# Performance work log

Hardware: AMD Instinct MI355X
Metric: run time of the kernel (lower is better)

Reference implementation:

```python
import jax, jax.numpy as jnp
import numpy as np


def setup_inputs() -> dict:
    key = jax.random.key(0)
    k1, k2 = jax.random.split(key)
    inputs = jax.random.normal(k1, (16, 4096, 512), dtype=jnp.float32)
    # torch init is uniform(-1/num_codes, 1/num_codes); match scale
    codebooks = jax.random.uniform(k2, (4, 1024, 512), dtype=jnp.float32,
                                   minval=-1.0 / 1024, maxval=1.0 / 1024)
    return {"inputs": inputs, "codebooks": codebooks}


def _vq_level(flat, codebook):
    # flat: [N, D], codebook: [K, D]
    dists = (jnp.sum(flat * flat, axis=1, keepdims=True)
             + jnp.sum(codebook * codebook, axis=1)
             - 2.0 * jnp.matmul(flat, codebook.T))  # [N, K]
    idx = jnp.argmin(dists, axis=1)                  # [N]
    quantized = codebook[idx]                         # [N, D]
    return quantized, idx


def reference(inputs, codebooks):
    sg = jax.lax.stop_gradient
    num_levels = codebooks.shape[0]
    shp = inputs.shape
    D = shp[-1]
    flat_in = inputs.reshape(-1, D)

    residual = flat_in
    total_q = jnp.zeros_like(flat_in)
    all_idx = []
    total_q_loss = jnp.float32(0.0)
    total_e_loss = jnp.float32(0.0)
    for lvl in range(num_levels):
        quantized, idx = _vq_level(residual, codebooks[lvl])
        q_loss = jnp.mean((quantized - sg(residual)) ** 2)
        e_loss = jnp.mean((sg(quantized) - residual) ** 2)
        all_idx.append(idx.reshape(shp[:-1]))
        total_q = total_q + quantized
        total_q_loss = total_q_loss + q_loss
        total_e_loss = total_e_loss + e_loss
        residual = residual - sg(quantized)

    total_q = total_q.reshape(shp)
    final_ste = inputs + sg(total_q - inputs)
    return (final_ste,
            total_q_loss / num_levels,
            total_e_loss / num_levels,
            jnp.stack(all_idx, axis=0))
```

## Files before the change

kernel.cpp:

```cpp
#include <hip/hip_runtime.h>


#define NROWS 65536
#define DDIM  512
#define KC    1024

#define AS1 __attribute__((address_space(1)))
#define AS3 __attribute__((address_space(3)))

typedef __attribute__((ext_vector_type(8))) short short8v;
typedef __attribute__((ext_vector_type(4))) float f32x4;

__device__ __forceinline__ unsigned short f2bf(float f) {
  unsigned u = __float_as_uint(f);
  unsigned r = (u + 0x7FFFu + ((u >> 16) & 1u)) >> 16;
  return (unsigned short)r;
}

__device__ __forceinline__ bool lexlt(float v1, int i1, float v2, int i2) {
  return (v1 < v2) || (v1 == v2 && i1 < i2);
}

__device__ __forceinline__ void merge3(float& v0, float& v1, float& v2,
                                       float m0, float m1, float m2) {
  float x1 = fmaxf(v0, m0); v0 = fminf(v0, m0);
  float y = fminf(v1, m1), z = fmaxf(v1, m1);
  float nv1 = fminf(x1, y);
  v2 = fminf(fmaxf(x1, y), fminf(z, fminf(v2, m2)));
  v1 = nv1;
}

__device__ __forceinline__ void top3of4(float k0, float k1, float k2, float k3,
                                        float& m0, float& m1, float& m2) {
  float a = fminf(k0, k1), b = fmaxf(k0, k1);
  float c = fminf(k2, k3), d = fmaxf(k2, k3);
  m0 = fminf(a, c);
  float f = fmaxf(a, c), g = fminf(b, d);
  m1 = fminf(f, g); m2 = fmaxf(f, g);
}

__device__ __forceinline__ void wg_barrier() {
  asm volatile("" ::: "memory");
  __builtin_amdgcn_s_barrier();
  asm volatile("" ::: "memory");
}


__global__ void cnorm_kernel(const float* __restrict__ cbs,
                             float* __restrict__ cn32) {
  const int code = blockIdx.x;
  const int l = threadIdx.x;
  if (l >= 32) return;
  const int b = l >> 3, j = l & 7;
  const float* p = cbs + (size_t)code * DDIM + b * 128 + j;
  float racc;
  {
    #pragma clang fp contract(off)
    float x0 = p[0];
    racc = x0 * x0;
    for (int s = 1; s < 16; ++s) { float x = p[8 * s]; float sq = x * x; racc = racc + sq; }
  }
  {
    #pragma clang fp contract(off)
    float o;
    o = __shfl_xor(racc, 1, 64);  racc = racc + o;
    o = __shfl_xor(racc, 2, 64);  racc = racc + o;
    o = __shfl_xor(racc, 4, 64);  racc = racc + o;
    o = __shfl_xor(racc, 8, 64);  racc = racc + o;
    o = __shfl_xor(racc, 16, 64); racc = racc + o;
    if (l == 0) cn32[code] = racc;
  }
}

__global__ void cvt_bf16_kernel(const float4* __restrict__ in4,
                                ushort4* __restrict__ o4, long n4) {
  for (long i = blockIdx.x * (long)blockDim.x + threadIdx.x; i < n4;
       i += (long)gridDim.x * blockDim.x) {
    float4 v = in4[i];
    ushort4 o; o.x = f2bf(v.x); o.y = f2bf(v.y); o.z = f2bf(v.z); o.w = f2bf(v.w);
    o4[i] = o;
  }
}

__global__ void __launch_bounds__(256)
resupd_kernel(const float4* __restrict__ x4, const float* __restrict__ cbs,
              const float* __restrict__ idx_f, ushort4* __restrict__ res4,
              int nlev) {
  const int gwave = (blockIdx.x * 256 + threadIdx.x) >> 6;
  const int lane  = threadIdx.x & 63;
  const int nwaves = gridDim.x * 4;
  const float4* cb4 = (const float4*)cbs;
  for (int row = gwave; row < NROWS; row += nwaves) {
    int ci[4];
    for (int l = 0; l < nlev; ++l) ci[l] = (int)idx_f[(size_t)l * NROWS + row];
    #pragma unroll
    for (int half = 0; half < 2; ++half) {
      const int p = half * 64 + lane;
      float4 v = x4[(size_t)row * 128 + p];
      for (int l = 0; l < nlev; ++l) {
        const float4 c = cb4[((size_t)(l * KC + ci[l])) * 128 + p];
        v.x -= c.x; v.y -= c.y; v.z -= c.z; v.w -= c.w;
      }
      ushort4 o; o.x = f2bf(v.x); o.y = f2bf(v.y); o.z = f2bf(v.z); o.w = f2bf(v.w);
      res4[(size_t)row * 128 + p] = o;
    }
  }
}

template <int LVL>
__global__ void __launch_bounds__(256, 4)
score_gemm(const ushort* __restrict__ res, const ushort* __restrict__ cbb,
           const float* __restrict__ cn32, float* __restrict__ partials) {
  __shared__ ushort At[2][128 * 32];
  __shared__ ushort Bt[2][128 * 32];
  __shared__ float halfTop[2][2][64][3];

  const int t = threadIdx.x;
  const int w = t >> 6, lane = t & 63;
  const int fr = lane & 15, kg = lane >> 4;
  const int rh = w >> 1, ch = w & 1;
  const int xcd = blockIdx.x & 7;
  const int j   = blockIdx.x >> 3;
  const int colTile = j & 7;
  const int rowTile = xcd * 64 + (j >> 3);
  const int row0 = rowTile * 128;

  const ushort* Asrc = res + (size_t)row0 * DDIM;
  const ushort* Bsrc = cbb + ((size_t)LVL * KC + colTile * 128) * DDIM;

  const int r0s = t >> 2, kq = t & 3;
  const int r1s = 64 + r0s;
  const size_t off0 = (size_t)r0s * DDIM + (size_t)((kq ^ (r0s & 3)) * 8);
  const size_t off1 = (size_t)r1s * DDIM + (size_t)((kq ^ (r1s & 3)) * 8);
  const int kgs = (kg ^ (fr & 3)) * 8;

  f32x4 acc[4][4];
  #pragma unroll
  for (int ri = 0; ri < 4; ++ri)
    #pragma unroll
    for (int ci = 0; ci < 4; ++ci) { f32x4 z = {0.f, 0.f, 0.f, 0.f}; acc[ri][ci] = z; }

#define STG(KS, BI)                                                           \
  do {                                                                        \
    __builtin_amdgcn_global_load_lds(                                         \
        (const AS1 unsigned*)(Asrc + off0 + (KS) * 32),                       \
        (AS3 unsigned*)&At[BI][w * 512], 16, 0, 0);                           \
    __builtin_amdgcn_global_load_lds(                                         \
        (const AS1 unsigned*)(Asrc + off1 + (KS) * 32),                       \
        (AS3 unsigned*)&At[BI][2048 + w * 512], 16, 0, 0);                    \
    __builtin_amdgcn_global_load_lds(                                         \
        (const AS1 unsigned*)(Bsrc + off0 + (KS) * 32),                       \
        (AS3 unsigned*)&Bt[BI][w * 512], 16, 0, 0);                           \
    __builtin_amdgcn_global_load_lds(                                         \
        (const AS1 unsigned*)(Bsrc + off1 + (KS) * 32),                       \
        (AS3 unsigned*)&Bt[BI][2048 + w * 512], 16, 0, 0);                    \
  } while (0)

  STG(0, 0);
  #pragma unroll
  for (int ks = 0; ks < 16; ++ks) {
    const int cur = ks & 1;
    if (ks < 15) {
      STG(ks + 1, !cur);
      asm volatile("s_waitcnt vmcnt(4)" ::: "memory");
    } else {
      asm volatile("s_waitcnt vmcnt(0)" ::: "memory");
    }
    wg_barrier();
    short8v a[4], b[4];
    #pragma unroll
    for (int i = 0; i < 4; ++i)
      a[i] = *(const short8v*)&At[cur][(rh * 64 + i * 16 + fr) * 32 + kgs];
    #pragma unroll
    for (int i = 0; i < 4; ++i)
      b[i] = *(const short8v*)&Bt[cur][(ch * 64 + i * 16 + fr) * 32 + kgs];
    __builtin_amdgcn_s_setprio(1);
    #pragma unroll
    for (int ri = 0; ri < 4; ++ri)
      #pragma unroll
      for (int ci = 0; ci < 4; ++ci)
        acc[ri][ci] = __builtin_amdgcn_mfma_f32_16x16x32_bf16(
            a[ri], b[ci], acc[ri][ci], 0, 0, 0);
    __builtin_amdgcn_s_setprio(0);
    wg_barrier();
  }
#undef STG

  float cnv[4];
  #pragma unroll
  for (int ci = 0; ci < 4; ++ci)
    cnv[ci] = cn32[LVL * KC + colTile * 128 + ch * 64 + ci * 16 + fr] + 0.25f;

  #pragma unroll
  for (int ri = 0; ri < 4; ++ri) {
    #pragma unroll
    for (int j2 = 0; j2 < 4; ++j2) {
      float k[4];
      #pragma unroll
      for (int ci = 0; ci < 4; ++ci) {
        float s = fmaf(-2.0f, acc[ri][ci][j2], cnv[ci]);
        unsigned col = (unsigned)(colTile * 128 + ch * 64 + ci * 16 + fr);
        unsigned u = (__float_as_uint(s) & 0xFFFFFC00u) | col;
        k[ci] = __uint_as_float(u);
      }
      float m0, m1, m2;
      top3of4(k[0], k[1], k[2], k[3], m0, m1, m2);
      #pragma unroll
      for (int m = 1; m <= 8; m <<= 1) {
        float t0 = __shfl_xor(m0, m, 64);
        float t1 = __shfl_xor(m1, m, 64);
        float t2 = __shfl_xor(m2, m, 64);
        merge3(m0, m1, m2, t0, t1, t2);
      }
      if (fr == 0) {
        int row64 = ri * 16 + kg * 4 + j2;
        halfTop[rh][ch][row64][0] = m0;
        halfTop[rh][ch][row64][1] = m1;
        halfTop[rh][ch][row64][2] = m2;
      }
    }
  }
  __syncthreads();

  if (t < 128) {
    const int lrh = t >> 6, r64 = t & 63;
    float u0 = halfTop[lrh][0][r64][0], u1 = halfTop[lrh][0][r64][1],
          u2 = halfTop[lrh][0][r64][2];
    float s0 = halfTop[lrh][1][r64][0], s1 = halfTop[lrh][1][r64][1],
          s2 = halfTop[lrh][1][r64][2];
    merge3(u0, u1, u2, s0, s1, s2);
    const int grow = row0 + lrh * 64 + r64;
    partials[(size_t)(colTile * 3 + 0) * NROWS + grow] = u0;
    partials[(size_t)(colTile * 3 + 1) * NROWS + grow] = u1;
    partials[(size_t)(colTile * 3 + 2) * NROWS + grow] = u2;
  }
}

__global__ void __launch_bounds__(256)
combine_kernel(const float* __restrict__ partials, float* __restrict__ idx_io,
               int* __restrict__ qcnt, int* __restrict__ qrows,
               int* __restrict__ qcand, int LVL) {
  const int row = blockIdx.x * 256 + threadIdx.x;
  float v0 = 3.4e38f, v1 = 3.4e38f, v2 = 3.4e38f, v3 = 3.4e38f;
  #pragma unroll
  for (int p = 0; p < 24; ++p) {
    const float kv = partials[(size_t)p * NROWS + row];
    const bool b3 = kv < v3, b2 = kv < v2, b1 = kv < v1, b0 = kv < v0;
    v3 = b3 ? (b2 ? v2 : kv) : v3;
    v2 = b2 ? (b1 ? v1 : kv) : v2;
    v1 = b1 ? (b0 ? v0 : kv) : v1;
    v0 = b0 ? kv : v0;
  }
  if (v1 - v0 > 1e-3f) {
    idx_io[(size_t)LVL * NROWS + row] = (float)(__float_as_uint(v0) & 1023u);
  } else {
    int pos = atomicAdd(qcnt, 1);
    qrows[pos] = row;
    qcand[pos * 4 + 0] = (int)(__float_as_uint(v0) & 1023u);
    qcand[pos * 4 + 1] = (int)(__float_as_uint(v1) & 1023u);
    qcand[pos * 4 + 2] = (int)(__float_as_uint(v2) & 1023u);
    qcand[pos * 4 + 3] = (int)(__float_as_uint(v3) & 1023u);
  }
}

template <int LVL>
__global__ void __launch_bounds__(256, 2)
refine_kernel(const float* __restrict__ x, const float* __restrict__ cbs,
              const float* __restrict__ cn32, float* __restrict__ idx_io,
              const int* __restrict__ qcnt, const int* __restrict__ qrows,
              const int* __restrict__ qcand) {
  __shared__ float resf[32][516];
  __shared__ float vfinL[32][4];
  const int t = threadIdx.x;
  const int qn = *qcnt;
  const float4* x4  = (const float4*)x;
  const float4* cb4 = (const float4*)cbs;
  const float*  cnL = cn32 + LVL * KC;

  for (int base = blockIdx.x * 32; base < qn; base += gridDim.x * 32) {
    const int nn = min(32, qn - base);
    for (int sI = t; sI < nn * 128; sI += 256) {
      int lr = sI >> 7, q = sI & 127;
      int grow = qrows[base + lr];
      float4 v = x4[(size_t)grow * 128 + q];
      #pragma unroll
      for (int l = 0; l < LVL; ++l) {
        int ci = (int)idx_io[(size_t)l * NROWS + grow];
        float4 c = cb4[((size_t)(l * KC + ci)) * 128 + q];
        v.x -= c.x; v.y -= c.y; v.z -= c.z; v.w -= c.w;
      }
      *(float4*)(&resf[lr][q * 4]) = v;
    }
    __syncthreads();
    if (t < 128) {
      const int lr = t >> 2, cd = t & 3;
      if (lr < nn) {
        const int ci = qcand[(base + lr) * 4 + cd];
        float Bk[4];
        #pragma unroll
        for (int b = 0; b < 4; ++b) {
          #pragma clang fp contract(off)
          float racc[8];
          #pragma unroll
          for (int j = 0; j < 8; ++j) {
            float e = resf[lr][b * 128 + j]; racc[j] = e * e;
          }
          for (int s = 1; s < 16; ++s) {
            #pragma unroll
            for (int j = 0; j < 8; ++j) {
              float e = resf[lr][b * 128 + s * 8 + j];
              float sq = e * e; racc[j] = racc[j] + sq;
            }
          }
          float t0 = (racc[0] + racc[1]) + (racc[2] + racc[3]);
          float t1 = (racc[4] + racc[5]) + (racc[6] + racc[7]);
          Bk[b] = t0 + t1;
        }
        float Arow;
        {
          #pragma clang fp contract(off)
          Arow = (Bk[0] + Bk[1]) + (Bk[2] + Bk[3]);
        }
        const float4* cq = cb4 + ((size_t)LVL * KC + ci) * 128;
        float dacc = 0.0f;
        for (int q = 0; q < 128; ++q) {
          const float4 cv = cq[q];
          dacc = fmaf(resf[lr][q * 4 + 0], cv.x, dacc);
          dacc = fmaf(resf[lr][q * 4 + 1], cv.y, dacc);
          dacc = fmaf(resf[lr][q * 4 + 2], cv.z, dacc);
          dacc = fmaf(resf[lr][q * 4 + 3], cv.w, dacc);
        }
        float vfin;
        {
          #pragma clang fp contract(off)
          float ab = Arow + cnL[ci];
          vfin = ab - 2.0f * dacc;
        }
        vfinL[lr][cd] = vfin;
      }
    }
    __syncthreads();
    if (t < nn) {
      float bv = vfinL[t][0]; int bi = qcand[(base + t) * 4 + 0];
      #pragma unroll
      for (int cd = 1; cd < 4; ++cd) {
        float v = vfinL[t][cd]; int ii = qcand[(base + t) * 4 + cd];
        if (lexlt(v, ii, bv, bi)) { bv = v; bi = ii; }
      }
      idx_io[(size_t)LVL * NROWS + qrows[base + t]] = (float)bi;
    }
    __syncthreads();
  }
}

__global__ void __launch_bounds__(256)
finalize_kernel(const float4* __restrict__ x4, const float* __restrict__ cbs,
                const float* __restrict__ idx_f, float4* __restrict__ out,
                double* __restrict__ loss_acc) {
  double ls0 = 0.0, ls1 = 0.0, ls2 = 0.0, ls3 = 0.0;
  const int gwave = (blockIdx.x * 256 + threadIdx.x) >> 6;
  const int lane  = threadIdx.x & 63;
  const int nwaves = gridDim.x * 4;
  const float4* cb4 = (const float4*)cbs;

  for (int row = gwave; row < NROWS; row += nwaves) {
    int ci[4];
    #pragma unroll
    for (int l = 0; l < 4; ++l) ci[l] = (int)idx_f[(size_t)l * NROWS + row];
    #pragma unroll
    for (int half = 0; half < 2; ++half) {
      const int p = half * 64 + lane;
      const float4 xv = x4[(size_t)row * 128 + p];
      float4 rr = xv;
      float4 tq = make_float4(0.f, 0.f, 0.f, 0.f);
      #pragma unroll
      for (int l = 0; l < 4; ++l) {
        const float4 qv = cb4[((size_t)(l * KC + ci[l])) * 128 + p];
        rr.x -= qv.x; rr.y -= qv.y; rr.z -= qv.z; rr.w -= qv.w;
        const double ss = (double)rr.x * rr.x + (double)rr.y * rr.y +
                          (double)rr.z * rr.z + (double)rr.w * rr.w;
        if      (l == 0) ls0 += ss;
        else if (l == 1) ls1 += ss;
        else if (l == 2) ls2 += ss;
        else             ls3 += ss;
        tq.x += qv.x; tq.y += qv.y; tq.z += qv.z; tq.w += qv.w;
      }
      float4 o;
      o.x = xv.x + (tq.x - xv.x);
      o.y = xv.y + (tq.y - xv.y);
      o.z = xv.z + (tq.z - xv.z);
      o.w = xv.w + (tq.w - xv.w);
      out[(size_t)row * 128 + p] = o;
    }
  }
  #pragma unroll
  for (int m = 1; m <= 32; m <<= 1) {
    ls0 += __shfl_xor(ls0, m, 64);
    ls1 += __shfl_xor(ls1, m, 64);
    ls2 += __shfl_xor(ls2, m, 64);
    ls3 += __shfl_xor(ls3, m, 64);
  }
  __shared__ double sred[4][4];
  const int wave = threadIdx.x >> 6;
  if ((threadIdx.x & 63) == 0) {
    sred[wave][0] = ls0; sred[wave][1] = ls1; sred[wave][2] = ls2; sred[wave][3] = ls3;
  }
  __syncthreads();
  if (threadIdx.x < 4) {
    const double v = sred[0][threadIdx.x] + sred[1][threadIdx.x] +
                     sred[2][threadIdx.x] + sred[3][threadIdx.x];
    atomicAdd(loss_acc + threadIdx.x, v);
  }
}

__global__ void write_losses_kernel(const double* __restrict__ loss_acc,
                                    float* __restrict__ out) {
  if (threadIdx.x == 0 && blockIdx.x == 0) {
    const double inv = 1.0 / (double)((size_t)NROWS * (size_t)DDIM);
    const double tv = (loss_acc[0] * inv + loss_acc[1] * inv +
                       loss_acc[2] * inv + loss_acc[3] * inv) * 0.25;
    out[33554432] = (float)tv;
    out[33554433] = (float)tv;
  }
}

extern "C" void kernel_launch(void* const* d_in, const int* in_sizes, int n_in,
                              void* d_out, int out_size, void* d_ws, size_t ws_size,
                              hipStream_t stream) {
  (void)in_sizes; (void)n_in; (void)out_size; (void)ws_size;
  const float* x   = (const float*)d_in[0];
  const float* cbs = (const float*)d_in[1];
  float* out_f     = (float*)d_out;
  float* idx_f     = out_f + 33554434;

  ushort* cbb  = (ushort*)d_ws;
  ushort* res  = (ushort*)((char*)d_ws + 4194304);
  float*  cn32 = (float*)((char*)d_ws + 4194304 + 67108864);
  double* loss = (double*)((char*)d_ws + 4194304 + 67108864 + 16384);

  float* partials = out_f;
  int*   qcnt  = (int*)(out_f + 1572864);
  int*   qrows = (int*)(out_f + 1572868);
  int*   qcand = (int*)(out_f + 1638404);

  hipMemsetAsync(loss, 0, 4 * sizeof(double), stream);
  hipMemsetAsync(qcnt, 0, 4 * sizeof(int), stream);

  cnorm_kernel<<<4096, 64, 0, stream>>>(cbs, cn32);
  cvt_bf16_kernel<<<2048, 256, 0, stream>>>((const float4*)cbs, (ushort4*)cbb,
                                            (long)4 * KC * DDIM / 4);
  resupd_kernel<<<2048, 256, 0, stream>>>((const float4*)x, cbs, idx_f,
                                          (ushort4*)res, 0);

  score_gemm<0><<<4096, 256, 0, stream>>>(res, cbb, cn32, partials);
  combine_kernel<<<256, 256, 0, stream>>>(partials, idx_f, qcnt + 0, qrows, qcand, 0);
  refine_kernel<0><<<512, 256, 0, stream>>>(x, cbs, cn32, idx_f, qcnt + 0, qrows, qcand);
  resupd_kernel<<<2048, 256, 0, stream>>>((const float4*)x, cbs, idx_f,
                                          (ushort4*)res, 1);

  score_gemm<1><<<4096, 256, 0, stream>>>(res, cbb, cn32, partials);
  combine_kernel<<<256, 256, 0, stream>>>(partials, idx_f, qcnt + 1, qrows, qcand, 1);
  refine_kernel<1><<<512, 256, 0, stream>>>(x, cbs, cn32, idx_f, qcnt + 1, qrows, qcand);
  resupd_kernel<<<2048, 256, 0, stream>>>((const float4*)x, cbs, idx_f,
                                          (ushort4*)res, 2);

  score_gemm<2><<<4096, 256, 0, stream>>>(res, cbb, cn32, partials);
  combine_kernel<<<256, 256, 0, stream>>>(partials, idx_f, qcnt + 2, qrows, qcand, 2);
  refine_kernel<2><<<512, 256, 0, stream>>>(x, cbs, cn32, idx_f, qcnt + 2, qrows, qcand);
  resupd_kernel<<<2048, 256, 0, stream>>>((const float4*)x, cbs, idx_f,
                                          (ushort4*)res, 3);

  score_gemm<3><<<4096, 256, 0, stream>>>(res, cbb, cn32, partials);
  combine_kernel<<<256, 256, 0, stream>>>(partials, idx_f, qcnt + 3, qrows, qcand, 3);
  refine_kernel<3><<<512, 256, 0, stream>>>(x, cbs, cn32, idx_f, qcnt + 3, qrows, qcand);

  finalize_kernel<<<2048, 256, 0, stream>>>((const float4*)x, cbs, idx_f,
                                            (float4*)d_out, loss);
  write_losses_kernel<<<1, 64, 0, stream>>>(loss, out_f);
}
```

Baseline: 1.106 ms.

## Enlarge score GEMM tile to 256x128 with triple-buffered LDS pipeline

The score GEMM block tile grows from 128x128 to 256x128. Each wave now computes a 128x64 sub-tile with 8x4 MFMA accumulators, which raises arithmetic intensity and halves how often codebook tiles are reloaded. LDS staging moves from double to triple buffering with a single barrier per k-step and a new swizzle, and the grid is halved to match. The cost is higher register pressure (launch bounds drop to 2 blocks per SIMD) and lower occupancy.

```diff
diff --git a/kernel.cpp b/kernel.cpp
--- a/kernel.cpp
+++ b/kernel.cpp
@@ -107,101 +107,101 @@
   }
 }
 
+#define SLOTU 12288
+
 template <int LVL>
-__global__ void __launch_bounds__(256, 4)
+__global__ void __launch_bounds__(256, 2)
 score_gemm(const ushort* __restrict__ res, const ushort* __restrict__ cbb,
            const float* __restrict__ cn32, float* __restrict__ partials) {
-  __shared__ ushort At[2][128 * 32];
-  __shared__ ushort Bt[2][128 * 32];
-  __shared__ float halfTop[2][2][64][3];
+  __shared__ ushort lds[3 * SLOTU];
 
   const int t = threadIdx.x;
-  const int w = t >> 6, lane = t & 63;
-  const int fr = lane & 15, kg = lane >> 4;
-  const int rh = w >> 1, ch = w & 1;
+  const int w = t >> 6, l = t & 63;
+  const int fr = l & 15, kg = l >> 4;
+  const int wm = w >> 1, wn = w & 1;
   const int xcd = blockIdx.x & 7;
   const int j   = blockIdx.x >> 3;
   const int colTile = j & 7;
-  const int rowTile = xcd * 64 + (j >> 3);
-  const int row0 = rowTile * 128;
+  const int rowTile = xcd * 32 + (j >> 3);
+  const int row0 = rowTile * 256;
 
   const ushort* Asrc = res + (size_t)row0 * DDIM;
   const ushort* Bsrc = cbb + ((size_t)LVL * KC + colTile * 128) * DDIM;
 
-  const int r0s = t >> 2, kq = t & 3;
-  const int r1s = 64 + r0s;
-  const size_t off0 = (size_t)r0s * DDIM + (size_t)((kq ^ (r0s & 3)) * 8);
-  const size_t off1 = (size_t)r1s * DDIM + (size_t)((kq ^ (r1s & 3)) * 8);
-  const int kgs = (kg ^ (fr & 3)) * 8;
-
-  f32x4 acc[4][4];
-  #pragma unroll
-  for (int ri = 0; ri < 4; ++ri)
-    #pragma unroll
-    for (int ci = 0; ci < 4; ++ci) { f32x4 z = {0.f, 0.f, 0.f, 0.f}; acc[ri][ci] = z; }
-
-#define STG(KS, BI)                                                           \
+  const int ch = (t & 3) ^ ((t >> 3) & 3);
+  const size_t aoff = (size_t)(t >> 2) * DDIM + (size_t)(ch * 8);
+
+  const int slr = kg ^ ((fr >> 1) & 3);
+  const int rdA = (wm * 128 + fr) * 32 + slr * 8;
+  const int rdB = (wn * 64 + fr) * 32 + slr * 8;
+
+  f32x4 acc[8][4];
+  #pragma unroll
+  for (int mi = 0; mi < 8; ++mi)
+    #pragma unroll
+    for (int ni = 0; ni < 4; ++ni) { f32x4 z = {0.f, 0.f, 0.f, 0.f}; acc[mi][ni] = z; }
+
+#define STG(KS, S)                                                            \
   do {                                                                        \
-    __builtin_amdgcn_global_load_lds(                                         \
-        (const AS1 unsigned*)(Asrc + off0 + (KS) * 32),                       \
-        (AS3 unsigned*)&At[BI][w * 512], 16, 0, 0);                           \
-    __builtin_amdgcn_global_load_lds(                                         \
-        (const AS1 unsigned*)(Asrc + off1 + (KS) * 32),                       \
-        (AS3 unsigned*)&At[BI][2048 + w * 512], 16, 0, 0);                    \
-    __builtin_amdgcn_global_load_lds(                                         \
-        (const AS1 unsigned*)(Bsrc + off0 + (KS) * 32),                       \
-        (AS3 unsigned*)&Bt[BI][w * 512], 16, 0, 0);                           \
-    __builtin_amdgcn_global_load_lds(                                         \
-        (const AS1 unsigned*)(Bsrc + off1 + (KS) * 32),                       \
-        (AS3 unsigned*)&Bt[BI][2048 + w * 512], 16, 0, 0);                    \
+    _Pragma("unroll")                                                         \
+    for (int i = 0; i < 4; ++i)                                               \
+      __builtin_amdgcn_global_load_lds(                                       \
+          (const AS1 unsigned*)(Asrc + aoff + (size_t)i * 64 * DDIM + (KS) * 32), \
+          (AS3 unsigned*)&lds[(S) * SLOTU + (i * 256 + t) * 8], 16, 0, 0);    \
+    _Pragma("unroll")                                                         \
+    for (int i = 0; i < 2; ++i)                                               \
+      __builtin_amdgcn_global_load_lds(                                       \
+          (const AS1 unsigned*)(Bsrc + aoff + (size_t)i * 64 * DDIM + (KS) * 32), \
+          (AS3 unsigned*)&lds[(S) * SLOTU + 8192 + (i * 256 + t) * 8], 16, 0, 0); \
   } while (0)
 
   STG(0, 0);
   #pragma unroll
   for (int ks = 0; ks < 16; ++ks) {
-    const int cur = ks & 1;
+    const int s = ks % 3;
     if (ks < 15) {
-      STG(ks + 1, !cur);
-      asm volatile("s_waitcnt vmcnt(4)" ::: "memory");
+      STG(ks + 1, (ks + 1) % 3);
+      asm volatile("s_waitcnt vmcnt(6)" ::: "memory");
     } else {
       asm volatile("s_waitcnt vmcnt(0)" ::: "memory");
     }
     wg_barrier();
-    short8v a[4], b[4];
-    #pragma unroll
-    for (int i = 0; i < 4; ++i)
-      a[i] = *(const short8v*)&At[cur][(rh * 64 + i * 16 + fr) * 32 + kgs];
-    #pragma unroll
-    for (int i = 0; i < 4; ++i)
-      b[i] = *(const short8v*)&Bt[cur][(ch * 64 + i * 16 + fr) * 32 + kgs];
+    short8v a[8], b[4];
+    #pragma unroll
+    for (int ni = 0; ni < 4; ++ni)
+      b[ni] = *(const short8v*)&lds[s * SLOTU + 8192 + rdB + ni * 512];
+    #pragma unroll
+    for (int mi = 0; mi < 8; ++mi)
+      a[mi] = *(const short8v*)&lds[s * SLOTU + rdA + mi * 512];
     __builtin_amdgcn_s_setprio(1);
     #pragma unroll
-    for (int ri = 0; ri < 4; ++ri)
-      #pragma unroll
-      for (int ci = 0; ci < 4; ++ci)
-        acc[ri][ci] = __builtin_amdgcn_mfma_f32_16x16x32_bf16(
-            a[ri], b[ci], acc[ri][ci], 0, 0, 0);
+    for (int mi = 0; mi < 8; ++mi)
+      #pragma unroll
+      for (int ni = 0; ni < 4; ++ni)
+        acc[mi][ni] = __builtin_amdgcn_mfma_f32_16x16x32_bf16(
+            a[mi], b[ni], acc[mi][ni], 0, 0, 0);
     __builtin_amdgcn_s_setprio(0);
-    wg_barrier();
   }
 #undef STG
-
+  __syncthreads();
+
+  float* hT = (float*)lds;
   float cnv[4];
   #pragma unroll
-  for (int ci = 0; ci < 4; ++ci)
-    cnv[ci] = cn32[LVL * KC + colTile * 128 + ch * 64 + ci * 16 + fr] + 0.25f;
-
-  #pragma unroll
-  for (int ri = 0; ri < 4; ++ri) {
+  for (int ni = 0; ni < 4; ++ni)
+    cnv[ni] = cn32[LVL * KC + colTile * 128 + wn * 64 + ni * 16 + fr] + 0.25f;
+
+  #pragma unroll
+  for (int mi = 0; mi < 8; ++mi) {
     #pragma unroll
     for (int j2 = 0; j2 < 4; ++j2) {
       float k[4];
       #pragma unroll
-      for (int ci = 0; ci < 4; ++ci) {
-        float s = fmaf(-2.0f, acc[ri][ci][j2], cnv[ci]);
-        unsigned col = (unsigned)(colTile * 128 + ch * 64 + ci * 16 + fr);
+      for (int ni = 0; ni < 4; ++ni) {
+        float s = fmaf(-2.0f, acc[mi][ni][j2], cnv[ni]);
+        unsigned col = (unsigned)(colTile * 128 + wn * 64 + ni * 16 + fr);
         unsigned u = (__float_as_uint(s) & 0xFFFFFC00u) | col;
-        k[ci] = __uint_as_float(u);
+        k[ni] = __uint_as_float(u);
       }
       float m0, m1, m2;
       top3of4(k[0], k[1], k[2], k[3], m0, m1, m2);
@@ -213,23 +213,25 @@
         merge3(m0, m1, m2, t0, t1, t2);
       }
       if (fr == 0) {
-        int row64 = ri * 16 + kg * 4 + j2;
-        halfTop[rh][ch][row64][0] = m0;
-        halfTop[rh][ch][row64][1] = m1;
-        halfTop[rh][ch][row64][2] = m2;
+        int r128 = mi * 16 + kg * 4 + j2;
+        hT[(((wm * 2 + wn) * 128) + r128) * 3 + 0] = m0;
+        hT[(((wm * 2 + wn) * 128) + r128) * 3 + 1] = m1;
+        hT[(((wm * 2 + wn) * 128) + r128) * 3 + 2] = m2;
       }
     }
   }
   __syncthreads();
 
-  if (t < 128) {
-    const int lrh = t >> 6, r64 = t & 63;
-    float u0 = halfTop[lrh][0][r64][0], u1 = halfTop[lrh][0][r64][1],
-          u2 = halfTop[lrh][0][r64][2];
-    float s0 = halfTop[lrh][1][r64][0], s1 = halfTop[lrh][1][r64][1],
-          s2 = halfTop[lrh][1][r64][2];
+  {
+    const int lwm = t >> 7, r128 = t & 127;
+    float u0 = hT[(((lwm * 2 + 0) * 128) + r128) * 3 + 0];
+    float u1 = hT[(((lwm * 2 + 0) * 128) + r128) * 3 + 1];
+    float u2 = hT[(((lwm * 2 + 0) * 128) + r128) * 3 + 2];
+    float s0 = hT[(((lwm * 2 + 1) * 128) + r128) * 3 + 0];
+    float s1 = hT[(((lwm * 2 + 1) * 128) + r128) * 3 + 1];
+    float s2 = hT[(((lwm * 2 + 1) * 128) + r128) * 3 + 2];
     merge3(u0, u1, u2, s0, s1, s2);
-    const int grow = row0 + lrh * 64 + r64;
+    const int grow = row0 + t;
     partials[(size_t)(colTile * 3 + 0) * NROWS + grow] = u0;
     partials[(size_t)(colTile * 3 + 1) * NROWS + grow] = u1;
     partials[(size_t)(colTile * 3 + 2) * NROWS + grow] = u2;
@@ -452,25 +454,25 @@
   resupd_kernel<<<2048, 256, 0, stream>>>((const float4*)x, cbs, idx_f,
                                           (ushort4*)res, 0);
 
-  score_gemm<0><<<4096, 256, 0, stream>>>(res, cbb, cn32, partials);
+  score_gemm<0><<<2048, 256, 0, stream>>>(res, cbb, cn32, partials);
   combine_kernel<<<256, 256, 0, stream>>>(partials, idx_f, qcnt + 0, qrows, qcand, 0);
   refine_kernel<0><<<512, 256, 0, stream>>>(x, cbs, cn32, idx_f, qcnt + 0, qrows, qcand);
   resupd_kernel<<<2048, 256, 0, stream>>>((const float4*)x, cbs, idx_f,
                                           (ushort4*)res, 1);
 
-  score_gemm<1><<<4096, 256, 0, stream>>>(res, cbb, cn32, partials);
+  score_gemm<1><<<2048, 256, 0, stream>>>(res, cbb, cn32, partials);
   combine_kernel<<<256, 256, 0, stream>>>(partials, idx_f, qcnt + 1, qrows, qcand, 1);
   refine_kernel<1><<<512, 256, 0, stream>>>(x, cbs, cn32, idx_f, qcnt + 1, qrows, qcand);
   resupd_kernel<<<2048, 256, 0, stream>>>((const float4*)x, cbs, idx_f,
                                           (ushort4*)res, 2);
 
-  score_gemm<2><<<4096, 256, 0, stream>>>(res, cbb, cn32, partials);
+  score_gemm<2><<<2048, 256, 0, stream>>>(res, cbb, cn32, partials);
   combine_kernel<<<256, 256, 0, stream>>>(partials, idx_f, qcnt + 2, qrows, qcand, 2);
   refine_kernel<2><<<512, 256, 0, stream>>>(x, cbs, cn32, idx_f, qcnt + 2, qrows, qcand);
   resupd_kernel<<<2048, 256, 0, stream>>>((const float4*)x, cbs, idx_f,
                                           (ushort4*)res, 3);
 
-  score_gemm<3><<<4096, 256, 0, stream>>>(res, cbb, cn32, partials);
+  score_gemm<3><<<2048, 256, 0, stream>>>(res, cbb, cn32, partials);
   combine_kernel<<<256, 256, 0, stream>>>(partials, idx_f, qcnt + 3, qrows, qcand, 3);
   refine_kernel<3><<<512, 256, 0, stream>>>(x, cbs, cn32, idx_f, qcnt + 3, qrows, qcand);
 
```

New measurement: 1.208 ms. +9.2%, slower.

## Refine candidates with one thread per candidate and change LDS swizzle in score GEMM

Applied to the files above, without the earlier changes.

The refine kernel no longer stages a 32-row fp32 residual tile in LDS with block barriers. Each thread now handles one (row, candidate) pair: it recomputes the residual straight from global x and the earlier codebook rows, accumulates the norm and dot product in registers, and picks the argmin across the 4 lanes with wave shuffles. The grid is doubled to 1024 blocks. Separately, the score GEMM's LDS XOR swizzle changes from row-based to thread-group-based, which is meant to reduce bank conflicts. The cost is redundant global reads, since each of the 4 candidate threads recomputes the same residual.

```diff
diff --git a/kernel.cpp b/kernel.cpp
--- a/kernel.cpp
+++ b/kernel.cpp
@@ -130,9 +130,10 @@
 
   const int r0s = t >> 2, kq = t & 3;
   const int r1s = 64 + r0s;
-  const size_t off0 = (size_t)r0s * DDIM + (size_t)((kq ^ (r0s & 3)) * 8);
-  const size_t off1 = (size_t)r1s * DDIM + (size_t)((kq ^ (r1s & 3)) * 8);
-  const int kgs = (kg ^ (fr & 3)) * 8;
+  const int swz = (t >> 3) & 3;
+  const size_t off0 = (size_t)r0s * DDIM + (size_t)((kq ^ swz) * 8);
+  const size_t off1 = (size_t)r1s * DDIM + (size_t)((kq ^ swz) * 8);
+  const int kgs = (kg ^ ((fr >> 1) & 3)) * 8;
 
   f32x4 acc[4][4];
   #pragma unroll
@@ -264,92 +265,83 @@
 }
 
 template <int LVL>
-__global__ void __launch_bounds__(256, 2)
+__global__ void __launch_bounds__(256)
 refine_kernel(const float* __restrict__ x, const float* __restrict__ cbs,
               const float* __restrict__ cn32, float* __restrict__ idx_io,
               const int* __restrict__ qcnt, const int* __restrict__ qrows,
               const int* __restrict__ qcand) {
-  __shared__ float resf[32][516];
-  __shared__ float vfinL[32][4];
-  const int t = threadIdx.x;
   const int qn = *qcnt;
   const float4* x4  = (const float4*)x;
   const float4* cb4 = (const float4*)cbs;
   const float*  cnL = cn32 + LVL * KC;
 
-  for (int base = blockIdx.x * 32; base < qn; base += gridDim.x * 32) {
-    const int nn = min(32, qn - base);
-    for (int sI = t; sI < nn * 128; sI += 256) {
-      int lr = sI >> 7, q = sI & 127;
-      int grow = qrows[base + lr];
-      float4 v = x4[(size_t)grow * 128 + q];
-      #pragma unroll
-      for (int l = 0; l < LVL; ++l) {
-        int ci = (int)idx_io[(size_t)l * NROWS + grow];
-        float4 c = cb4[((size_t)(l * KC + ci)) * 128 + q];
-        v.x -= c.x; v.y -= c.y; v.z -= c.z; v.w -= c.w;
-      }
-      *(float4*)(&resf[lr][q * 4]) = v;
-    }
-    __syncthreads();
-    if (t < 128) {
-      const int lr = t >> 2, cd = t & 3;
-      if (lr < nn) {
-        const int ci = qcand[(base + lr) * 4 + cd];
-        float Bk[4];
+  for (int wi = blockIdx.x * 256 + threadIdx.x; wi < qn * 4;
+       wi += gridDim.x * 256) {
+    const int qi = wi >> 2, cd = wi & 3;
+    const int grow = qrows[qi];
+    const int ci   = qcand[qi * 4 + cd];
+    const float4* xr = x4 + (size_t)grow * 128;
+    const float4* cq = cb4 + ((size_t)LVL * KC + ci) * 128;
+    const float4* cl[LVL > 0 ? LVL : 1];
+    #pragma unroll
+    for (int l = 0; l < LVL; ++l)
+      cl[l] = cb4 +
+              ((size_t)(l * KC + (int)idx_io[(size_t)l * NROWS + grow])) * 128;
+
+    float Bk[4];
+    float dacc = 0.0f;
+    #pragma unroll
+    for (int b = 0; b < 4; ++b) {
+      #pragma clang fp contract(off)
+      float racc[8];
+      for (int s = 0; s < 16; ++s) {
+        const int q = b * 32 + s * 2;
+        float4 v0 = xr[q], v1 = xr[q + 1];
         #pragma unroll
-        for (int b = 0; b < 4; ++b) {
-          #pragma clang fp contract(off)
-          float racc[8];
-          #pragma unroll
-          for (int j = 0; j < 8; ++j) {
-            float e = resf[lr][b * 128 + j]; racc[j] = e * e;
-          }
-          for (int s = 1; s < 16; ++s) {
-            #pragma unroll
-            for (int j = 0; j < 8; ++j) {
-              float e = resf[lr][b * 128 + s * 8 + j];
-              float sq = e * e; racc[j] = racc[j] + sq;
-            }
-          }
-          float t0 = (racc[0] + racc[1]) + (racc[2] + racc[3]);
-          float t1 = (racc[4] + racc[5]) + (racc[6] + racc[7]);
-          Bk[b] = t0 + t1;
+        for (int l = 0; l < LVL; ++l) {
+          const float4 c0 = cl[l][q], c1 = cl[l][q + 1];
+          v0.x -= c0.x; v0.y -= c0.y; v0.z -= c0.z; v0.w -= c0.w;
+          v1.x -= c1.x; v1.y -= c1.y; v1.z -= c1.z; v1.w -= c1.w;
         }
-        float Arow;
-        {
-          #pragma clang fp contract(off)
-          Arow = (Bk[0] + Bk[1]) + (Bk[2] + Bk[3]);
+        if (s == 0) {
+          racc[0] = v0.x * v0.x; racc[1] = v0.y * v0.y;
+          racc[2] = v0.z * v0.z; racc[3] = v0.w * v0.w;
+          racc[4] = v1.x * v1.x; racc[5] = v1.y * v1.y;
+          racc[6] = v1.z * v1.z; racc[7] = v1.w * v1.w;
+        } else {
+          float sq;
+          sq = v0.x * v0.x; racc[0] = racc[0] + sq;
+          sq = v0.y * v0.y; racc[1] = racc[1] + sq;
+          sq = v0.z * v0.z; racc[2] = racc[2] + sq;
+          sq = v0.w * v0.w; racc[3] = racc[3] + sq;
+          sq = v1.x * v1.x; racc[4] = racc[4] + sq;
+          sq = v1.y * v1.y; racc[5] = racc[5] + sq;
+          sq = v1.z * v1.z; racc[6] = racc[6] + sq;
+          sq = v1.w * v1.w; racc[7] = racc[7] + sq;
         }
-        const float4* cq = cb4 + ((size_t)LVL * KC + ci) * 128;
-        float dacc = 0.0f;
-        for (int q = 0; q < 128; ++q) {
-          const float4 cv = cq[q];
-          dacc = fmaf(resf[lr][q * 4 + 0], cv.x, dacc);
-          dacc = fmaf(resf[lr][q * 4 + 1], cv.y, dacc);
-          dacc = fmaf(resf[lr][q * 4 + 2], cv.z, dacc);
-          dacc = fmaf(resf[lr][q * 4 + 3], cv.w, dacc);
-        }
-        float vfin;
-        {
-          #pragma clang fp contract(off)
-          float ab = Arow + cnL[ci];
-          vfin = ab - 2.0f * dacc;
-        }
-        vfinL[lr][cd] = vfin;
-      }
-    }
-    __syncthreads();
-    if (t < nn) {
-      float bv = vfinL[t][0]; int bi = qcand[(base + t) * 4 + 0];
-      #pragma unroll
-      for (int cd = 1; cd < 4; ++cd) {
-        float v = vfinL[t][cd]; int ii = qcand[(base + t) * 4 + cd];
-        if (lexlt(v, ii, bv, bi)) { bv = v; bi = ii; }
-      }
-      idx_io[(size_t)LVL * NROWS + qrows[base + t]] = (float)bi;
-    }
-    __syncthreads();
+        const float4 c0 = cq[q], c1 = cq[q + 1];
+        dacc = fmaf(v0.x, c0.x, dacc); dacc = fmaf(v0.y, c0.y, dacc);
+        dacc = fmaf(v0.z, c0.z, dacc); dacc = fmaf(v0.w, c0.w, dacc);
+        dacc = fmaf(v1.x, c1.x, dacc); dacc = fmaf(v1.y, c1.y, dacc);
+        dacc = fmaf(v1.z, c1.z, dacc); dacc = fmaf(v1.w, c1.w, dacc);
+      }
+      float t0 = (racc[0] + racc[1]) + (racc[2] + racc[3]);
+      float t1 = (racc[4] + racc[5]) + (racc[6] + racc[7]);
+      Bk[b] = t0 + t1;
+    }
+    float vfin;
+    {
+      #pragma clang fp contract(off)
+      float Arow = (Bk[0] + Bk[1]) + (Bk[2] + Bk[3]);
+      float ab = Arow + cnL[ci];
+      vfin = ab - 2.0f * dacc;
+    }
+    float bv = vfin; int bi = ci;
+    float ov = __shfl_xor(bv, 1, 64); int oi = __shfl_xor(bi, 1, 64);
+    if (lexlt(ov, oi, bv, bi)) { bv = ov; bi = oi; }
+    ov = __shfl_xor(bv, 2, 64); oi = __shfl_xor(bi, 2, 64);
+    if (lexlt(ov, oi, bv, bi)) { bv = ov; bi = oi; }
+    if (cd == 0) idx_io[(size_t)LVL * NROWS + grow] = (float)bi;
   }
 }
 
@@ -454,25 +446,25 @@
 
   score_gemm<0><<<4096, 256, 0, stream>>>(res, cbb, cn32, partials);
   combine_kernel<<<256, 256, 0, stream>>>(partials, idx_f, qcnt + 0, qrows, qcand, 0);
-  refine_kernel<0><<<512, 256, 0, stream>>>(x, cbs, cn32, idx_f, qcnt + 0, qrows, qcand);
+  refine_kernel<0><<<1024, 256, 0, stream>>>(x, cbs, cn32, idx_f, qcnt + 0, qrows, qcand);
   resupd_kernel<<<2048, 256, 0, stream>>>((const float4*)x, cbs, idx_f,
                                           (ushort4*)res, 1);
 
   score_gemm<1><<<4096, 256, 0, stream>>>(res, cbb, cn32, partials);
   combine_kernel<<<256, 256, 0, stream>>>(partials, idx_f, qcnt + 1, qrows, qcand, 1);
-  refine_kernel<1><<<512, 256, 0, stream>>>(x, cbs, cn32, idx_f, qcnt + 1, qrows, qcand);
+  refine_kernel<1><<<1024, 256, 0, stream>>>(x, cbs, cn32, idx_f, qcnt + 1, qrows, qcand);
   resupd_kernel<<<2048, 256, 0, stream>>>((const float4*)x, cbs, idx_f,
                                           (ushort4*)res, 2);
 
   score_gemm<2><<<4096, 256, 0, stream>>>(res, cbb, cn32, partials);
   combine_kernel<<<256, 256, 0, stream>>>(partials, idx_f, qcnt + 2, qrows, qcand, 2);
-  refine_kernel<2><<<512, 256, 0, stream>>>(x, cbs, cn32, idx_f, qcnt + 2, qrows, qcand);
+  refine_kernel<2><<<1024, 256, 0, stream>>>(x, cbs, cn32, idx_f, qcnt + 2, qrows, qcand);
   resupd_kernel<<<2048, 256, 0, stream>>>((const float4*)x, cbs, idx_f,
                                           (ushort4*)res, 3);
 
   score_gemm<3><<<4096, 256, 0, stream>>>(res, cbb, cn32, partials);
   combine_kernel<<<256, 256, 0, stream>>>(partials, idx_f, qcnt + 3, qrows, qcand, 3);
-  refine_kernel<3><<<512, 256, 0, stream>>>(x, cbs, cn32, idx_f, qcnt + 3, qrows, qcand);
+  refine_kernel<3><<<1024, 256, 0, stream>>>(x, cbs, cn32, idx_f, qcnt + 3, qrows, qcand);
 
   finalize_kernel<<<2048, 256, 0, stream>>>((const float4*)x, cbs, idx_f,
                                             (float4*)d_out, loss);
```

New measurement: 960.3 us. 1.15x faster.
